# Performance work log

Hardware: AMD Instinct MI355X
Metric: run time of the kernel (lower is better)

## Reference

```python
import jax, jax.numpy as jnp
import numpy as np

B, T, H, L, V = 32, 512, 1024, 256, 13  # V = FDIM_JOINT_VOCAB_DECODING


def setup_inputs() -> dict:
    key = jax.random.key(0)
    ks = jax.random.split(key, 16)
    s_in = 1.0 / np.sqrt(V)
    s_h = 1.0 / np.sqrt(H)
    s_l = 1.0 / np.sqrt(L)
    s_hl = 1.0 / np.sqrt(H + L)
    # one-hot-like teacher-forced inputs (first token is all-zero start token)
    labels = jax.random.randint(ks[0], (B, T), 0, V)
    seq_input = jax.nn.one_hot(labels, V, dtype=jnp.float32)
    seq_input = jnp.concatenate([jnp.zeros((B, 1, V), jnp.float32), seq_input[:, :-1]], axis=1)
    lengths = jax.random.randint(ks[1], (B,), T // 2, T + 1).astype(jnp.int32)
    return {
        "seq_input": seq_input,
        "latent_vec": jax.random.normal(ks[2], (B, L), jnp.float32),
        "labels": labels.astype(jnp.int32),
        "lengths": lengths,
        "W_ih": jax.random.uniform(ks[3], (4 * H, V), jnp.float32, -s_h, s_h),
        "W_hh": jax.random.uniform(ks[4], (4 * H, H), jnp.float32, -s_h, s_h),
        "b_ih": jax.random.uniform(ks[5], (4 * H,), jnp.float32, -s_h, s_h),
        "b_hh": jax.random.uniform(ks[6], (4 * H,), jnp.float32, -s_h, s_h),
        "Wz": jax.random.uniform(ks[7], (H, L), jnp.float32, -s_l, s_l),
        "bz": jax.random.uniform(ks[8], (H,), jnp.float32, -s_l, s_l),
        "Wnl": jax.random.uniform(ks[9], (H, H + L), jnp.float32, -s_hl, s_hl),
        "bnl": jax.random.uniform(ks[10], (H,), jnp.float32, -s_hl, s_hl),
        "Wout": jax.random.uniform(ks[11], (V, H), jnp.float32, -s_h, s_h),
        "bout": jax.random.uniform(ks[12], (V,), jnp.float32, -s_h, s_h),
    }


def _forward(seq_input, latent_vec, labels, lengths,
             W_ih, W_hh, b_ih, b_hh, Wz, bz, Wnl, bnl, Wout, bout):
    h0 = jax.nn.relu(latent_vec @ Wz.T + bz)              # [B,H]
    c0 = jnp.zeros_like(h0)

    def step(carry, x_t):
        h, c = carry
        gates = x_t @ W_ih.T + b_ih + h @ W_hh.T + b_hh   # [B,4H]
        i, f, g, o = jnp.split(gates, 4, axis=-1)         # torch LSTMCell gate order
        c = jax.nn.sigmoid(f) * c + jax.nn.sigmoid(i) * jnp.tanh(g)
        h = jax.nn.sigmoid(o) * jnp.tanh(c)
        return (h, c), h

    xs = jnp.swapaxes(seq_input, 0, 1)                    # [T,B,V]
    _, hs = jax.lax.scan(step, (h0, c0), xs)              # [T,B,H]
    hs = jnp.swapaxes(hs, 0, 1)                           # [B,T,H]

    # aggregate: cat(h, z) -> relu(W_nonlinear) -> W
    lat = jnp.broadcast_to(latent_vec[:, None, :], (hs.shape[0], hs.shape[1], latent_vec.shape[-1]))
    feat = jnp.concatenate([hs, lat], axis=-1)            # [B,T,H+L]
    logits = jax.nn.relu(feat @ Wnl.T + bnl) @ Wout.T + bout  # [B,T,V]

    logp = jax.nn.log_softmax(logits, axis=-1)
    nll = -jnp.take_along_axis(logp, labels[..., None].astype(jnp.int32), axis=-1)[..., 0]  # [B,T]
    mask = (jnp.arange(T)[None, :] < lengths[:, None]).astype(nll.dtype)
    batch_loss = jnp.sum(nll * mask, axis=1)              # per-sequence segment sum
    return batch_loss


def reference(seq_input, latent_vec, labels, lengths,
              W_ih, W_hh, b_ih, b_hh, Wz, bz, Wnl, bnl, Wout, bout):
    batch_loss = _forward(seq_input, latent_vec, labels, lengths,
                          W_ih, W_hh, b_ih, b_hh, Wz, bz, Wnl, bnl, Wout, bout)
    return jnp.sum(batch_loss), batch_loss
```

## Files before the change

kernel.cpp:

```cpp
#include <hip/hip_runtime.h>
#include <hip/hip_bf16.h>

#define B_   32
#define T_   512
#define H_   1024
#define L_   256
#define V_   13
#define G4H  4096
#define KHL  1280

typedef float f32x4 __attribute__((ext_vector_type(4)));
typedef short s16x8 __attribute__((ext_vector_type(8)));
typedef unsigned short u16;
typedef unsigned int   u32;
typedef unsigned long long u64;

#define OFF_BF   33619968u
#define OFF_BF2  42008576u
#define OFF_AZ   44630016u
#define OFF_BAR  44646400u
#define OFF_MID  44650496u
#define OFF_GX   OFF_MID
#define OFF_TOK  (OFF_MID + 229376u)

__device__ __forceinline__ u16 f2bf(float f) {
    union { float f; u32 u; } v; v.f = f;
    u32 u = v.u;
    u32 r = (u + 0x7fffu + ((u >> 16) & 1u)) >> 16;
    return (u16)r;
}
__device__ __forceinline__ float bf2f(u16 h) {
    union { u32 u; float f; } v; v.u = ((u32)h) << 16;
    return v.f;
}
__device__ __forceinline__ float sigm_(float x) {
    x = fminf(fmaxf(x, -30.f), 30.f);
    return 1.f / (1.f + __expf(-x));
}
__device__ __forceinline__ float tanh_(float x) {
    x = fminf(fmaxf(x, -15.f), 15.f);
    float e = __expf(2.f * x);
    return (e - 1.f) / (e + 1.f);
}

__device__ __forceinline__ u32 afrag_pos(int bl, int k) {
    return (u32)((k >> 5) * 512 + ((bl | (((k >> 3) & 3) << 4)) << 3) + (k & 7));
}

__global__ __launch_bounds__(256) void k_init_misc(
        const float* __restrict__ latent, const float* __restrict__ Wz,
        const float* __restrict__ bz,
        u16* __restrict__ Ax, u16* __restrict__ Az, int* __restrict__ bar) {
    int gid = blockIdx.x * 256 + threadIdx.x;
    int b = gid >> 10, j = gid & 1023;
    const float* lrow = latent + b * L_;
    const float* wrow = Wz + j * L_;
    float acc = bz[j];
    #pragma unroll 4
    for (int l = 0; l < L_; ++l) acc += lrow[l] * wrow[l];
    Ax[(b >> 4) * 16384 + afrag_pos(b & 15, j)] = f2bf(fmaxf(acc, 0.f));
    if (gid < B_ * L_) {
        int bb = gid >> 8, l = gid & 255;
        Az[(bb >> 4) * 4096 + afrag_pos(bb & 15, l)] = f2bf(latent[gid]);
    }
    if (gid < 1024) bar[gid] = 0;
}

__global__ __launch_bounds__(256) void k_init_gx(
        const float* __restrict__ W_ih, const float* __restrict__ b_ih,
        const float* __restrict__ b_hh, float* __restrict__ Gx) {
    int row = blockIdx.x * 256 + threadIdx.x;
    if (row >= G4H) return;
    int gg = row >> 10, jg = row & 1023;
    float base = b_ih[row] + b_hh[row];
    float* d = Gx + (size_t)jg * 56;
    const float* wr = W_ih + (size_t)row * V_;
    #pragma unroll
    for (int t = 0; t < V_; ++t) d[t * 4 + gg] = base + wr[t];
    d[13 * 4 + gg] = base;
}

__global__ __launch_bounds__(256) void k_init_tok(
        const float* __restrict__ seq, u16* __restrict__ tok) {
    int gid = blockIdx.x * 256 + threadIdx.x;
    int s = gid >> 5, b = gid & 31;
    const float* r = seq + ((size_t)b * T_ + s) * V_;
    int t = 13;
    #pragma unroll
    for (int v = 0; v < V_; ++v) if (r[v] > 0.5f) t = v;
    tok[gid] = (u16)t;
}

__global__ __launch_bounds__(256) void k_init_wfrag(
        const float* __restrict__ W_hh, u16* __restrict__ Bf) {
    int base = blockIdx.x * 256 + threadIdx.x;
    #pragma unroll
    for (int i = 0; i < 8; ++i) {
        int idx = base + i * 524288;
        int jv   = idx & 7;
        int lane = (idx >> 3) & 63;
        int kc   = (idx >> 9) & 31;
        int nt   = idx >> 14;
        int u = lane & 15;
        int row = (u & 3) * H_ + nt * 4 + (u >> 2);
        int k = kc * 32 + (lane >> 4) * 8 + jv;
        Bf[idx] = f2bf(W_hh[row * H_ + k]);
    }
}

__global__ __launch_bounds__(256) void k_init_wfrag2(
        const float* __restrict__ Wnl, u16* __restrict__ Bf2) {
    int idx = blockIdx.x * 256 + threadIdx.x;
    for (; idx < 1310720; idx += 524288) {
        int jv   = idx & 7;
        int lane = (idx >> 3) & 63;
        int q    = idx >> 9;
        int kc   = q % 40;
        int nt2  = q / 40;
        int n = nt2 * 16 + (lane & 15);
        int k = kc * 32 + (lane >> 4) * 8 + jv;
        Bf2[idx] = f2bf(Wnl[n * KHL + k]);
    }
}

__global__ __launch_bounds__(512, 1) void k_recur(
        const u16* __restrict__ tokbuf, const float* __restrict__ Gx,
        const u16* __restrict__ Bf, u16* __restrict__ Ax,
        int* __restrict__ bar) {
    __shared__ uint4 AhV[2048];
    int tid = threadIdx.x;
    int bid = blockIdx.x;
    int mt = bid & 1;
    int p  = bid >> 1;
    int w = tid >> 6, L = tid & 63;
    int nt = p * 8 + w;
    int lm = L & 15, quad = L >> 4;

    s16x8 afr[32];
    {
        const u16* bfp = Bf + (size_t)nt * 16384 + L * 8;
        #pragma unroll
        for (int kc = 0; kc < 32; ++kc)
            afr[kc] = *reinterpret_cast<const s16x8*>(bfp + kc * 512);
    }
    int jg = nt * 4 + quad;
    int b = mt * 16 + lm;
    const float* gxp = Gx + (size_t)jg * 56;
    u32 posu16 = (u32)((nt >> 3) * 512 + ((lm | (((nt >> 1) & 3) << 4)) << 3)
                       + (nt & 1) * 4 + quad);
    int* flags = bar + mt * 512;
    const int* myflag = flags + (w + 8 * (L & 3)) * 16;
    u32* AxD = (u32*)Ax;
    float c = 0.f;

    for (int s = 0; s < T_; ++s) {
        int tok = tokbuf[s * 32 + b];
        float4 gx4 = *reinterpret_cast<const float4*>(gxp + tok * 4);

        for (;;) {
            int v = __hip_atomic_load(myflag, __ATOMIC_RELAXED,
                                      __HIP_MEMORY_SCOPE_AGENT);
            if (__all(v >= s)) break;
            __builtin_amdgcn_s_sleep(1);
        }
        const uint4* srcq = (const uint4*)((const char*)Ax
                             + ((size_t)s * 2 + mt) * 32768);
        #pragma unroll
        for (int i = 0; i < 4; ++i)
            AhV[i * 512 + tid] = srcq[i * 512 + tid];
        __syncthreads();

        f32x4 a0 = {0.f,0.f,0.f,0.f}, a1 = {0.f,0.f,0.f,0.f};
        f32x4 a2 = {0.f,0.f,0.f,0.f}, a3 = {0.f,0.f,0.f,0.f};
        const u16* hp = (const u16*)AhV + L * 8;
        #pragma unroll
        for (int kc = 0; kc < 32; kc += 4) {
            s16x8 h0 = *reinterpret_cast<const s16x8*>(hp + kc * 512);
            s16x8 h1 = *reinterpret_cast<const s16x8*>(hp + (kc + 1) * 512);
            s16x8 h2 = *reinterpret_cast<const s16x8*>(hp + (kc + 2) * 512);
            s16x8 h3 = *reinterpret_cast<const s16x8*>(hp + (kc + 3) * 512);
            a0 = __builtin_amdgcn_mfma_f32_16x16x32_bf16(afr[kc],     h0, a0, 0, 0, 0);
            a1 = __builtin_amdgcn_mfma_f32_16x16x32_bf16(afr[kc + 1], h1, a1, 0, 0, 0);
            a2 = __builtin_amdgcn_mfma_f32_16x16x32_bf16(afr[kc + 2], h2, a2, 0, 0, 0);
            a3 = __builtin_amdgcn_mfma_f32_16x16x32_bf16(afr[kc + 3], h3, a3, 0, 0, 0);
        }
        float gi = a0[0] + a1[0] + a2[0] + a3[0] + gx4.x;
        float gf = a0[1] + a1[1] + a2[1] + a3[1] + gx4.y;
        float gg = a0[2] + a1[2] + a2[2] + a3[2] + gx4.z;
        float go = a0[3] + a1[3] + a2[3] + a3[3] + gx4.w;
        float ig = sigm_(gi), fg = sigm_(gf);
        float gt = tanh_(gg), og = sigm_(go);
        c = fg * c + ig * gt;
        float hv = og * tanh_(c);

        u32 bits = (u32)f2bf(hv);
        u32 other = (u32)(u16)__shfl_xor((int)bits, 16);
        if (!(quad & 1)) {
            u32 word = bits | (other << 16);
            __hip_atomic_store(
                AxD + ((size_t)(s + 1) * 2 + mt) * 8192 + (posu16 >> 1),
                word, __ATOMIC_RELAXED, __HIP_MEMORY_SCOPE_AGENT);
        }
        if (s == T_ - 1) break;
        __syncthreads();
        if (tid == 0)
            __hip_atomic_store(flags + p * 16, s + 1, __ATOMIC_RELAXED,
                               __HIP_MEMORY_SCOPE_AGENT);
    }
}

__global__ __launch_bounds__(256) void k_gemm1(
        const u16* __restrict__ Ax, const u16* __restrict__ Az,
        const u16* __restrict__ Bf2, const float* __restrict__ bnl,
        u16* __restrict__ mid) {
    int tid = threadIdx.x;
    int nb = blockIdx.x;
    int mb = blockIdx.y;
    int w = tid >> 6, L = tid & 63;
    int lm = L & 15, quad = L >> 4;
    int mti0 = mb * 8 + w * 2;
    const u16* a0p = Ax + ((size_t)mti0 + 2) * 16384 + L * 8;
    const u16* a1p = a0p + 16384;
    const u16* az0 = Az + L * 8;
    const u16* az1 = az0 + 4096;
    const u16* bp = Bf2 + (size_t)(nb * 4) * 40 * 512 + L * 8;

    f32x4 acc[2][4];
    #pragma unroll
    for (int a = 0; a < 2; ++a)
        #pragma unroll
        for (int n = 0; n < 4; ++n) acc[a][n] = (f32x4){0.f, 0.f, 0.f, 0.f};

    #pragma unroll 4
    for (int kc = 0; kc < 32; ++kc) {
        s16x8 a0 = *reinterpret_cast<const s16x8*>(a0p + kc * 512);
        s16x8 a1 = *reinterpret_cast<const s16x8*>(a1p + kc * 512);
        #pragma unroll
        for (int n4 = 0; n4 < 4; ++n4) {
            s16x8 bv = *reinterpret_cast<const s16x8*>(bp + ((size_t)n4 * 40 + kc) * 512);
            acc[0][n4] = __builtin_amdgcn_mfma_f32_16x16x32_bf16(a0, bv, acc[0][n4], 0, 0, 0);
            acc[1][n4] = __builtin_amdgcn_mfma_f32_16x16x32_bf16(a1, bv, acc[1][n4], 0, 0, 0);
        }
    }
    #pragma unroll
    for (int kc2 = 0; kc2 < 8; ++kc2) {
        s16x8 a0 = *reinterpret_cast<const s16x8*>(az0 + kc2 * 512);
        s16x8 a1 = *reinterpret_cast<const s16x8*>(az1 + kc2 * 512);
        #pragma unroll
        for (int n4 = 0; n4 < 4; ++n4) {
            s16x8 bv = *reinterpret_cast<const s16x8*>(bp + ((size_t)n4 * 40 + 32 + kc2) * 512);
            acc[0][n4] = __builtin_amdgcn_mfma_f32_16x16x32_bf16(a0, bv, acc[0][n4], 0, 0, 0);
            acc[1][n4] = __builtin_amdgcn_mfma_f32_16x16x32_bf16(a1, bv, acc[1][n4], 0, 0, 0);
        }
    }
    #pragma unroll
    for (int mt2 = 0; mt2 < 2; ++mt2)
        #pragma unroll
        for (int n4 = 0; n4 < 4; ++n4)
            #pragma unroll
            for (int r = 0; r < 4; ++r) {
                int m = mb * 128 + w * 32 + mt2 * 16 + quad * 4 + r;
                int n = (nb * 4 + n4) * 16 + lm;
                float v = acc[mt2][n4][r] + bnl[n];
                mid[(size_t)m * H_ + n] = f2bf(fmaxf(v, 0.f));
            }
}

__global__ __launch_bounds__(256) void k_loss(
        const u16* __restrict__ mid, const float* __restrict__ Wout,
        const float* __restrict__ bout, const int* __restrict__ labels,
        const int* __restrict__ lengths, float* __restrict__ out) {
    int mrow = blockIdx.x;
    int b = mrow & 31, t = mrow >> 5;
    if (t >= lengths[b]) return;
    int tid = threadIdx.x;
    float p[V_];
    #pragma unroll
    for (int v = 0; v < V_; ++v) p[v] = 0.f;
    uint2 raw = *reinterpret_cast<const uint2*>(mid + (size_t)mrow * H_ + tid * 4);
    const u16* rs = (const u16*)&raw;
    float mv0 = bf2f(rs[0]), mv1 = bf2f(rs[1]), mv2 = bf2f(rs[2]), mv3 = bf2f(rs[3]);
    #pragma unroll
    for (int v = 0; v < V_; ++v) {
        float4 wv = *reinterpret_cast<const float4*>(Wout + v * H_ + tid * 4);
        p[v] = mv0 * wv.x + mv1 * wv.y + mv2 * wv.z + mv3 * wv.w;
    }
    #pragma unroll
    for (int off = 32; off > 0; off >>= 1)
        #pragma unroll
        for (int v = 0; v < V_; ++v) p[v] += __shfl_down(p[v], off);
    __shared__ float red[4][V_];
    int w = tid >> 6, L = tid & 63;
    if (L == 0)
        #pragma unroll
        for (int v = 0; v < V_; ++v) red[w][v] = p[v];
    __syncthreads();
    if (tid == 0) {
        float lg[V_]; float mx = -1e30f;
        #pragma unroll
        for (int v = 0; v < V_; ++v) {
            lg[v] = red[0][v] + red[1][v] + red[2][v] + red[3][v] + bout[v];
            mx = fmaxf(mx, lg[v]);
        }
        float se = 0.f;
        #pragma unroll
        for (int v = 0; v < V_; ++v) se += __expf(lg[v] - mx);
        float lse = mx + logf(se);
        int lab = labels[b * T_ + t];
        atomicAdd(&out[1 + b], lse - lg[lab]);
    }
}

__global__ void k_final(float* __restrict__ out) {
    float s = 0.f;
    for (int b = 0; b < B_; ++b) s += out[1 + b];
    out[0] = s;
}

extern "C" void kernel_launch(void* const* d_in, const int* in_sizes, int n_in,
                              void* d_out, int out_size, void* d_ws, size_t ws_size,
                              hipStream_t stream) {
    const float* seq    = (const float*)d_in[0];
    const float* latent = (const float*)d_in[1];
    const int*   labels = (const int*)d_in[2];
    const int*   lengths= (const int*)d_in[3];
    const float* W_ih   = (const float*)d_in[4];
    const float* W_hh   = (const float*)d_in[5];
    const float* b_ih   = (const float*)d_in[6];
    const float* b_hh   = (const float*)d_in[7];
    const float* Wz     = (const float*)d_in[8];
    const float* bz     = (const float*)d_in[9];
    const float* Wnl    = (const float*)d_in[10];
    const float* bnl    = (const float*)d_in[11];
    const float* Wout   = (const float*)d_in[12];
    const float* bout   = (const float*)d_in[13];

    char* ws = (char*)d_ws;
    u16*   Ax   = (u16*)(ws);
    u16*   Bf   = (u16*)(ws + OFF_BF);
    u16*   Bf2  = (u16*)(ws + OFF_BF2);
    u16*   Az   = (u16*)(ws + OFF_AZ);
    int*   bar  = (int*)(ws + OFF_BAR);
    u16*   mid  = (u16*)(ws + OFF_MID);
    float* Gx   = (float*)(ws + OFF_GX);
    u16*   tok  = (u16*)(ws + OFF_TOK);
    float* out  = (float*)d_out;

    hipMemsetAsync(d_out, 0, 33 * sizeof(float), stream);
    k_init_misc<<<128, 256, 0, stream>>>(latent, Wz, bz, Ax, Az, bar);
    k_init_gx<<<16, 256, 0, stream>>>(W_ih, b_ih, b_hh, Gx);
    k_init_tok<<<64, 256, 0, stream>>>(seq, tok);
    k_init_wfrag<<<2048, 256, 0, stream>>>(W_hh, Bf);
    k_init_wfrag2<<<2048, 256, 0, stream>>>(Wnl, Bf2);
    k_recur<<<64, 512, 0, stream>>>(tok, Gx, Bf, Ax, bar);
    k_gemm1<<<dim3(16, 128), 256, 0, stream>>>(Ax, Az, Bf2, bnl, mid);
    k_loss<<<16384, 256, 0, stream>>>(mid, Wout, bout, labels, lengths, out);
    k_final<<<1, 1, 0, stream>>>(out);
}
```

Baseline: 1.483 ms.

## Replace block barriers with per-wave flags and double-buffered LDS in LSTM recurrence

The persistent recurrence kernel now has each wave publish its own agent-scope flag after its h store, in place of a block-wide __syncthreads followed by a single per-block flag. Waves poll the per-wave flags and stage the h tile into a double-buffered LDS region, then sync within the workgroup through LDS flags. The aim is to cut barrier latency on the serial T=512 critical path. The cost is more flags to poll (8192 entries are zeroed) and subtler memory ordering, which rests on a relaxed store placed after s_waitcnt.

```diff
diff --git a/kernel.cpp b/kernel.cpp
--- a/kernel.cpp
+++ b/kernel.cpp
@@ -19,7 +19,7 @@
 #define OFF_BF2  42008576u
 #define OFF_AZ   44630016u
 #define OFF_BAR  44646400u
-#define OFF_MID  44650496u
+#define OFF_MID  44679168u
 #define OFF_GX   OFF_MID
 #define OFF_TOK  (OFF_MID + 229376u)
 
@@ -63,7 +63,7 @@
         int bb = gid >> 8, l = gid & 255;
         Az[(bb >> 4) * 4096 + afrag_pos(bb & 15, l)] = f2bf(latent[gid]);
     }
-    if (gid < 1024) bar[gid] = 0;
+    if (gid < 8192) bar[gid] = 0;
 }
 
 __global__ __launch_bounds__(256) void k_init_gx(
@@ -127,7 +127,8 @@
         const u16* __restrict__ tokbuf, const float* __restrict__ Gx,
         const u16* __restrict__ Bf, u16* __restrict__ Ax,
         int* __restrict__ bar) {
-    __shared__ uint4 AhV[2048];
+    __shared__ uint4 AhV[4096];
+    __shared__ int dsf[8];
     int tid = threadIdx.x;
     int bid = blockIdx.x;
     int mt = bid & 1;
@@ -136,6 +137,9 @@
     int nt = p * 8 + w;
     int lm = L & 15, quad = L >> 4;
 
+    if (tid < 8) dsf[tid] = 0;
+    __syncthreads();
+
     s16x8 afr[32];
     {
         const u16* bfp = Bf + (size_t)nt * 16384 + L * 8;
@@ -148,8 +152,9 @@
     const float* gxp = Gx + (size_t)jg * 56;
     u32 posu16 = (u32)((nt >> 3) * 512 + ((lm | (((nt >> 1) & 3) << 4)) << 3)
                        + (nt & 1) * 4 + quad);
-    int* flags = bar + mt * 512;
-    const int* myflag = flags + (w + 8 * (L & 3)) * 16;
+    const int* gpoll = bar + (((mt << 8) + ((w + 8 * ((L >> 3) & 3)) << 3)
+                               + (L & 7)) << 4);
+    int* myflag = bar + (((mt << 8) + nt) << 4);
     u32* AxD = (u32*)Ax;
     float c = 0.f;
 
@@ -157,32 +162,49 @@
         int tok = tokbuf[s * 32 + b];
         float4 gx4 = *reinterpret_cast<const float4*>(gxp + tok * 4);
 
+        if (s > 0) {
+            for (;;) {
+                int v = __hip_atomic_load(gpoll, __ATOMIC_RELAXED,
+                                          __HIP_MEMORY_SCOPE_AGENT);
+                if (__all(v >= s)) break;
+                __builtin_amdgcn_s_sleep(1);
+            }
+            asm volatile("" ::: "memory");
+        }
+        const uint4* src = (const uint4*)((const char*)Ax
+                            + ((size_t)s * 2 + mt) * 32768);
+        uint4* buf = AhV + (s & 1) * 2048;
+        uint4 r0 = src[(w     ) * 64 + L];
+        uint4 r1 = src[(w +  8) * 64 + L];
+        uint4 r2 = src[(w + 16) * 64 + L];
+        uint4 r3 = src[(w + 24) * 64 + L];
+        buf[(w     ) * 64 + L] = r0;
+        buf[(w +  8) * 64 + L] = r1;
+        buf[(w + 16) * 64 + L] = r2;
+        buf[(w + 24) * 64 + L] = r3;
+        if (L == 0)
+            __hip_atomic_store(&dsf[w], s + 1, __ATOMIC_RELEASE,
+                               __HIP_MEMORY_SCOPE_WORKGROUP);
         for (;;) {
-            int v = __hip_atomic_load(myflag, __ATOMIC_RELAXED,
-                                      __HIP_MEMORY_SCOPE_AGENT);
-            if (__all(v >= s)) break;
+            int v = __hip_atomic_load(&dsf[L & 7], __ATOMIC_ACQUIRE,
+                                      __HIP_MEMORY_SCOPE_WORKGROUP);
+            if (__all(v > s)) break;
             __builtin_amdgcn_s_sleep(1);
         }
-        const uint4* srcq = (const uint4*)((const char*)Ax
-                             + ((size_t)s * 2 + mt) * 32768);
-        #pragma unroll
-        for (int i = 0; i < 4; ++i)
-            AhV[i * 512 + tid] = srcq[i * 512 + tid];
-        __syncthreads();
 
         f32x4 a0 = {0.f,0.f,0.f,0.f}, a1 = {0.f,0.f,0.f,0.f};
         f32x4 a2 = {0.f,0.f,0.f,0.f}, a3 = {0.f,0.f,0.f,0.f};
-        const u16* hp = (const u16*)AhV + L * 8;
-        #pragma unroll
-        for (int kc = 0; kc < 32; kc += 4) {
-            s16x8 h0 = *reinterpret_cast<const s16x8*>(hp + kc * 512);
-            s16x8 h1 = *reinterpret_cast<const s16x8*>(hp + (kc + 1) * 512);
-            s16x8 h2 = *reinterpret_cast<const s16x8*>(hp + (kc + 2) * 512);
-            s16x8 h3 = *reinterpret_cast<const s16x8*>(hp + (kc + 3) * 512);
-            a0 = __builtin_amdgcn_mfma_f32_16x16x32_bf16(afr[kc],     h0, a0, 0, 0, 0);
-            a1 = __builtin_amdgcn_mfma_f32_16x16x32_bf16(afr[kc + 1], h1, a1, 0, 0, 0);
-            a2 = __builtin_amdgcn_mfma_f32_16x16x32_bf16(afr[kc + 2], h2, a2, 0, 0, 0);
-            a3 = __builtin_amdgcn_mfma_f32_16x16x32_bf16(afr[kc + 3], h3, a3, 0, 0, 0);
+        const u16* hp = (const u16*)buf + L * 8;
+        #pragma unroll
+        for (int q = 0; q < 8; ++q) {
+            s16x8 h0 = *reinterpret_cast<const s16x8*>(hp + (q     ) * 512);
+            s16x8 h1 = *reinterpret_cast<const s16x8*>(hp + (q +  8) * 512);
+            s16x8 h2 = *reinterpret_cast<const s16x8*>(hp + (q + 16) * 512);
+            s16x8 h3 = *reinterpret_cast<const s16x8*>(hp + (q + 24) * 512);
+            a0 = __builtin_amdgcn_mfma_f32_16x16x32_bf16(afr[q],      h0, a0, 0, 0, 0);
+            a1 = __builtin_amdgcn_mfma_f32_16x16x32_bf16(afr[q +  8], h1, a1, 0, 0, 0);
+            a2 = __builtin_amdgcn_mfma_f32_16x16x32_bf16(afr[q + 16], h2, a2, 0, 0, 0);
+            a3 = __builtin_amdgcn_mfma_f32_16x16x32_bf16(afr[q + 24], h3, a3, 0, 0, 0);
         }
         float gi = a0[0] + a1[0] + a2[0] + a3[0] + gx4.x;
         float gf = a0[1] + a1[1] + a2[1] + a3[1] + gx4.y;
@@ -202,9 +224,9 @@
                 word, __ATOMIC_RELAXED, __HIP_MEMORY_SCOPE_AGENT);
         }
         if (s == T_ - 1) break;
-        __syncthreads();
-        if (tid == 0)
-            __hip_atomic_store(flags + p * 16, s + 1, __ATOMIC_RELAXED,
+        asm volatile("s_waitcnt vmcnt(0)" ::: "memory");
+        if (L == 0)
+            __hip_atomic_store(myflag, s + 1, __ATOMIC_RELAXED,
                                __HIP_MEMORY_SCOPE_AGENT);
     }
 }
```

Measured after the change: 1.744 ms. +17.6%, slower.
